# Kernel optimization log

Hardware: AMD Instinct MI355X
Metric: run time of the kernel (lower is better)

The kernel has to match this reference:

```python
import jax, jax.numpy as jnp
import numpy as np

N, K, A, P = 8192, 32, 5, 64
RBF_BINS = 16
D_MIN, D_MAX = 0.0, 22.0
REL_CLIP = 32


def _rbf(d, d_min=D_MIN, d_max=D_MAX, bins=RBF_BINS):
    centers = jnp.linspace(d_min, d_max, bins)
    sigma = (d_max - d_min) / bins
    return jnp.exp(-(((d[..., None] - centers) / sigma) ** 2))


def _frames(pos):
    # pos: [N, A, 3]; atoms 0=N, 1=CA, 2=C -> Gram-Schmidt backbone frame
    t = pos[:, 1]
    v1 = pos[:, 2] - t
    v2 = pos[:, 0] - t
    e1 = v1 / (jnp.linalg.norm(v1, axis=-1, keepdims=True) + 1e-6)
    u2 = v2 - (v2 * e1).sum(-1, keepdims=True) * e1
    e2 = u2 / (jnp.linalg.norm(u2, axis=-1, keepdims=True) + 1e-6)
    e3 = jnp.cross(e1, e2)
    R = jnp.stack([e1, e2, e3], axis=-1)  # [N,3,3], columns are basis vectors
    return R, t


def setup_inputs() -> dict:
    key = jax.random.key(0)
    ks = jax.random.split(key, 20)
    pos = jax.random.normal(ks[0], (N, A, 3), dtype=jnp.float32) * 3.0
    dmap = jax.random.uniform(ks[1], (N, N), dtype=jnp.float32) * 30.0
    neighbours = jax.random.randint(ks[2], (N, K), 0, N)
    resi = jax.random.randint(ks[3], (N,), 0, 512)
    chain = jnp.sort(jax.random.randint(ks[4], (N,), 0, 4))
    batch = jnp.sort(jax.random.randint(ks[5], (N,), 0, 8))
    mask = jnp.ones((N,), jnp.float32)

    def lin(k, fan_in, fan_out):
        return jax.random.normal(k, (fan_in, fan_out), dtype=jnp.float32) / np.sqrt(fan_in)

    REL = 2 * REL_CLIP + 1
    params = dict(
        W_rel=lin(ks[6], REL, P),
        W_dmap=lin(ks[7], RBF_BINS, P),
        W_dist=lin(ks[8], A * A * RBF_BINS, P),
        W_dir=lin(ks[9], A * 3, P),
        W_rot=lin(ks[10], 9, P),
        W_vec=lin(ks[11], A * 3, P),
        ln_g=jnp.ones((P,), jnp.float32),
        ln_b=jnp.zeros((P,), jnp.float32),
        W1=lin(ks[12], P, 2 * P),
        b1=jnp.zeros((2 * P,), jnp.float32),
        W2=lin(ks[13], 2 * P, P),
        b2=jnp.zeros((P,), jnp.float32),
    )
    return dict(pos=pos, dmap=dmap, neighbours=neighbours, resi=resi,
                chain=chain, batch=batch, mask=mask, **params)


def reference(pos, dmap, neighbours, resi, chain, batch, mask,
              W_rel, W_dmap, W_dist, W_dir, W_rot, W_vec,
              ln_g, ln_b, W1, b1, W2, b2):
    idx = jnp.clip(neighbours, 0, None)                     # safe gather for -1 padding
    nb_valid = (neighbours != -1).astype(mask.dtype)
    pair_mask = mask[:, None] * mask[idx] * nb_valid        # [N,K]

    # --- sequence relative position (one-hot, masked to same chain & batch) ---
    rel = jnp.clip(resi[idx] - resi[:, None], -REL_CLIP, REL_CLIP) + REL_CLIP
    same = ((chain[idx] == chain[:, None]) & (batch[idx] == batch[:, None]))
    rel_feat = jax.nn.one_hot(rel, 2 * REL_CLIP + 1, dtype=pos.dtype) * same[..., None].astype(pos.dtype)
    pair = jnp.einsum('nkf,fp->nkp', rel_feat, W_rel)

    # --- gathered distance-map branch ---
    dmap_nb = dmap[jnp.arange(N)[:, None], idx]             # [N,K]
    dmap_feat = jnp.where(pair_mask[..., None] > 0, _rbf(dmap_nb), 0.0)
    pair += jnp.einsum('nkf,fp->nkp', dmap_feat, W_dmap)

    # --- geometric features from frames ---
    R, t = _frames(pos)                                     # [N,3,3], [N,3]
    pos_j = pos[idx]                                        # [N,K,A,3]

    # all-atom pairwise distances residue i vs neighbour j: [N,K,A,A]
    d = jnp.linalg.norm(pos[:, None, :, None, :] - pos_j[:, :, None, :, :], axis=-1)
    dist_feat = _rbf(d).reshape(N, K, A * A * RBF_BINS)
    pair += jnp.einsum('nkf,fp->nkp', dist_feat, W_dist)

    # neighbour atoms in local frame of residue i: R_i^T (x - t_i)
    rel_vec = jnp.einsum('nji,nkaj->nkai', R, pos_j - t[:, None, None, :])  # [N,K,A,3]
    dirs = rel_vec / (jnp.linalg.norm(rel_vec, axis=-1, keepdims=True) + 1e-6)
    pair += jnp.einsum('nkf,fp->nkp', dirs.reshape(N, K, A * 3), W_dir)
    pair += jnp.einsum('nkf,fp->nkp', (rel_vec / 10.0).reshape(N, K, A * 3), W_vec)

    # relative rotation R_i^T R_j flattened: [N,K,9]
    rot = jnp.einsum('nji,nkjl->nkil', R, R[idx]).reshape(N, K, 9)
    pair += jnp.einsum('nkf,fp->nkp', rot, W_rot)

    # --- LayerNorm ---
    mu = pair.mean(-1, keepdims=True)
    var = ((pair - mu) ** 2).mean(-1, keepdims=True)
    pair = ln_g * (pair - mu) / jnp.sqrt(var + 1e-5) + ln_b

    # --- MLP (2P hidden, gelu) ---
    h = jax.nn.gelu(jnp.einsum('nkp,ph->nkh', pair, W1) + b1)
    pair = jnp.einsum('nkh,hp->nkp', h, W2) + b2
    return pair, pair_mask
```

## Files before the change

### kernel.cpp

```cpp
#include <hip/hip_runtime.h>
#include <cstdint>
#include <cstddef>

#define NN 8192
#define KK 32

typedef __bf16 bf16x8 __attribute__((ext_vector_type(8)));
typedef float  f32x4  __attribute__((ext_vector_type(4)));

union U4B { uint4 u; bf16x8 h; };
__device__ __forceinline__ bf16x8 asbf(uint4 u){ U4B v; v.u = u; return v.h; }

__device__ __forceinline__ unsigned short ftobf16(float f){
  union { float f; unsigned int i; } v; v.f = f;
  unsigned int x = v.i;
  x += 0x7fffu + ((x >> 16) & 1u);
  return (unsigned short)(x >> 16);
}
__device__ __forceinline__ float fast_gelu(float x){
  float y = 0.7978845608028654f * (x + 0.044715f * x * x * x);
  float e = __expf(2.0f * y);
  float t = 1.0f - 2.0f / (e + 1.0f);
  return 0.5f * x * (1.0f + t);
}

struct Frame { float e[9]; float t[3]; };
__device__ __forceinline__ Frame calc_frame(const float* p){
  Frame fr;
  float tx=p[3], ty=p[4], tz=p[5];
  float v1x=p[6]-tx, v1y=p[7]-ty, v1z=p[8]-tz;
  float v2x=p[0]-tx, v2y=p[1]-ty, v2z=p[2]-tz;
  float n1 = sqrtf(v1x*v1x+v1y*v1y+v1z*v1z) + 1e-6f;
  float e1x=v1x/n1, e1y=v1y/n1, e1z=v1z/n1;
  float dp = v2x*e1x+v2y*e1y+v2z*e1z;
  float ux=v2x-dp*e1x, uy=v2y-dp*e1y, uz=v2z-dp*e1z;
  float n2 = sqrtf(ux*ux+uy*uy+uz*uz) + 1e-6f;
  float e2x=ux/n2, e2y=uy/n2, e2z=uz/n2;
  fr.e[0]=e1x; fr.e[1]=e1y; fr.e[2]=e1z;
  fr.e[3]=e2x; fr.e[4]=e2y; fr.e[5]=e2z;
  fr.e[6]=e1y*e2z - e1z*e2y;
  fr.e[7]=e1z*e2x - e1x*e2z;
  fr.e[8]=e1x*e2y - e1y*e2x;
  fr.t[0]=tx; fr.t[1]=ty; fr.t[2]=tz;
  return fr;
}

__global__ void prep_w(const float* __restrict__ W_dmap, const float* __restrict__ W_dist,
    const float* __restrict__ W_dir, const float* __restrict__ W_rot,
    const float* __restrict__ W_vec, const float* __restrict__ W1,
    const float* __restrict__ W2, unsigned short* __restrict__ ws)
{
  int idx = blockIdx.x*256 + threadIdx.x;
  if (idx < 64*488){
    int p = idx / 488, k = idx - p*488;
    float v = 0.0f;
    if      (k < 400) v = W_dist[k*64+p];
    else if (k < 416) v = W_dmap[(k-400)*64+p];
    else if (k < 431) v = W_dir[(k-416)*64+p];
    else if (k < 446) v = W_vec[(k-431)*64+p];
    else if (k < 455) v = W_rot[(k-446)*64+p];
    ws[idx] = ftobf16(v);
  } else if (idx < 64*488 + 128*64){
    int i = idx - 64*488; int j = i>>6, p = i&63;
    ws[idx] = ftobf16(W1[p*128+j]);
  } else if (idx < 64*488 + 128*64 + 64*128){
    int i = idx - (64*488 + 128*64); int p = i>>7, j = i&127;
    ws[idx] = ftobf16(W2[j*64+p]);
  }
}

__global__ __launch_bounds__(256, 2)
void dsd_mfma(const float* __restrict__ pos, const float* __restrict__ dmap,
    const int* __restrict__ nbr, const int* __restrict__ resi,
    const int* __restrict__ chain, const int* __restrict__ batch,
    const float* __restrict__ mask,
    const float* __restrict__ W_rel,
    const float* __restrict__ ln_g, const float* __restrict__ ln_b,
    const float* __restrict__ b1, const float* __restrict__ b2,
    const unsigned short* __restrict__ wt,
    const unsigned short* __restrict__ w1t,
    const unsigned short* __restrict__ w2t,
    float* __restrict__ out)
{
  __shared__ __align__(16) unsigned short sFeat[32][488];
  __shared__ __align__(16) unsigned short sXA[32][72];
  __shared__ __align__(16) unsigned short sH[32][136];
  __shared__ __align__(16) float x32[32][68];
  __shared__ float sPosJ[32][16];
  __shared__ float sD[32][25];
  __shared__ float sPosI[15];
  __shared__ float sFrN[12];
  __shared__ float sLnG[64], sLnB[64], sB1[128], sB2[64];
  __shared__ int   sJ[32], sRel[32];
  __shared__ float sSame[32], sPm[32], sDv[32];

  const int tid  = threadIdx.x;
  const int w    = tid >> 6;
  const int lane = tid & 63;
  const int l15  = lane & 15;
  const int q    = lane >> 4;
  const int n    = blockIdx.x;
  const int mt   = w & 1;
  const int ng   = w >> 1;

  uint4 pB[15];
  {
    const unsigned short* rowp = wt + (size_t)(w*16 + l15)*488 + q*8;
    #pragma unroll
    for (int kk=0; kk<15; ++kk) pB[kk] = *(const uint4*)(rowp + kk*32);
  }
  uint4 b1B[4][2];
  #pragma unroll
  for (int t=0;t<4;++t){
    const unsigned short* rowp = w1t + (size_t)((ng*4+t)*16 + l15)*64 + q*8;
    #pragma unroll
    for (int kk=0;kk<2;++kk) b1B[t][kk] = *(const uint4*)(rowp + kk*32);
  }
  uint4 b2B[2][4];
  #pragma unroll
  for (int t=0;t<2;++t){
    const unsigned short* rowp = w2t + (size_t)((ng*2+t)*16 + l15)*128 + q*8;
    #pragma unroll
    for (int kk=0;kk<4;++kk) b2B[t][kk] = *(const uint4*)(rowp + kk*32);
  }

  if (tid < 32){
    int nb = nbr[n*KK + tid];
    int valid = (nb != -1) ? 1 : 0;
    int j = nb < 0 ? 0 : nb;
    sJ[tid] = j;
    int rl = resi[j] - resi[n];
    rl = rl < -32 ? -32 : (rl > 32 ? 32 : rl);
    sRel[tid] = rl + 32;
    sSame[tid] = (chain[j]==chain[n] && batch[j]==batch[n]) ? 1.0f : 0.0f;
    float pm = mask[n]*mask[j]*(float)valid;
    sPm[tid] = pm;
    sDv[tid] = dmap[(size_t)n*NN + j];
    out[(size_t)NN*KK*64 + (size_t)n*KK + tid] = pm;
  } else if (tid < 47){
    sPosI[tid-32] = pos[n*15 + (tid-32)];
  } else if (tid == 47){
    float pl[9];
    #pragma unroll
    for (int i=0;i<9;++i) pl[i] = pos[n*15+i];
    Frame fr = calc_frame(pl);
    #pragma unroll
    for (int i=0;i<9;++i) sFrN[i] = fr.e[i];
    #pragma unroll
    for (int i=0;i<3;++i) sFrN[9+i] = fr.t[i];
  } else if (tid >= 64 && tid < 192){
    sB1[tid-64] = b1[tid-64];
  } else if (tid >= 192){
    sB2[tid-192] = b2[tid-192];
  }
  if (tid < 64){ sLnG[tid] = ln_g[tid]; sLnB[tid] = ln_b[tid]; }
  __syncthreads();

  #pragma unroll
  for (int t=0;t<2;++t){
    int e = tid + t*256;
    int pair = e >> 4, qq = e & 15;
    if (qq < 15) sPosJ[pair][qq] = pos[sJ[pair]*15 + qq];
  }
  float wr0[4], wr1[4];
  #pragma unroll
  for (int r=0;r<4;++r){
    int p0 = q*4+r, p1 = 16+q*4+r;
    int pc = w*16 + l15;
    wr0[r] = (sSame[p0] != 0.0f) ? W_rel[sRel[p0]*64 + pc] : 0.0f;
    wr1[r] = (sSame[p1] != 0.0f) ? W_rel[sRel[p1]*64 + pc] : 0.0f;
  }
  __syncthreads();

  {
    int pair = tid >> 3, a = tid & 7;
    if (a < 5){
      float x0 = sPosJ[pair][a*3+0] - sFrN[9];
      float x1 = sPosJ[pair][a*3+1] - sFrN[10];
      float x2 = sPosJ[pair][a*3+2] - sFrN[11];
      float r0 = sFrN[0]*x0 + sFrN[1]*x1 + sFrN[2]*x2;
      float r1 = sFrN[3]*x0 + sFrN[4]*x1 + sFrN[5]*x2;
      float r2 = sFrN[6]*x0 + sFrN[7]*x1 + sFrN[8]*x2;
      float inv = 1.0f/(sqrtf(r0*r0+r1*r1+r2*r2)+1e-6f);
      sFeat[pair][416+a*3+0] = ftobf16(r0*inv);
      sFeat[pair][416+a*3+1] = ftobf16(r1*inv);
      sFeat[pair][416+a*3+2] = ftobf16(r2*inv);
      sFeat[pair][431+a*3+0] = ftobf16(r0*0.1f);
      sFeat[pair][431+a*3+1] = ftobf16(r1*0.1f);
      sFeat[pair][431+a*3+2] = ftobf16(r2*0.1f);
    }
  }
  if (tid < 32){
    Frame fj = calc_frame(sPosJ[tid]);
    #pragma unroll
    for (int i=0;i<3;++i)
      #pragma unroll
      for (int l=0;l<3;++l)
        sFeat[tid][446+i*3+l] = ftobf16(
          sFrN[i*3+0]*fj.e[l*3+0] + sFrN[i*3+1]*fj.e[l*3+1] + sFrN[i*3+2]*fj.e[l*3+2]);
  }
  #pragma unroll
  for (int t=0;t<4;++t){
    int e = tid + t*256;
    int pair = e >> 5, ab = e & 31;
    if (ab < 25){
      int a = ab/5, b = ab - (ab/5)*5;
      float dx = sPosI[a*3+0] - sPosJ[pair][b*3+0];
      float dy = sPosI[a*3+1] - sPosJ[pair][b*3+1];
      float dz = sPosI[a*3+2] - sPosJ[pair][b*3+2];
      sD[pair][ab] = sqrtf(dx*dx+dy*dy+dz*dz);
      sFeat[pair][455+ab] = 0;
    }
  }
  __syncthreads();

  for (int t=0;t<25;++t){
    int e = tid + t*256;
    int pair = e / 200;
    int rem  = e - pair*200;
    int ab = rem >> 3, cp = rem & 7;
    float d = sD[pair][ab];
    float z0 = (d - (float)(2*cp  )*(22.0f/15.0f)) * (1.0f/1.375f);
    float z1 = (d - (float)(2*cp+1)*(22.0f/15.0f)) * (1.0f/1.375f);
    unsigned int u0 = ftobf16(__expf(-z0*z0));
    unsigned int u1 = ftobf16(__expf(-z1*z1));
    *(unsigned int*)&sFeat[pair][ab*16 + cp*2] = u0 | (u1<<16);
  }
  #pragma unroll
  for (int t=0;t<2;++t){
    int e = tid + t*256;
    int pair = e >> 4, c = e & 15;
    float z = (sDv[pair] - (float)c*(22.0f/15.0f)) * (1.0f/1.375f);
    float v = (sPm[pair] > 0.0f) ? __expf(-z*z) : 0.0f;
    sFeat[pair][400+c] = ftobf16(v);
  }
  __syncthreads();

  f32x4 acc0 = {0.f,0.f,0.f,0.f}, acc1 = {0.f,0.f,0.f,0.f};
  {
    const unsigned short* a0p = &sFeat[l15][q*8];
    const unsigned short* a1p = &sFeat[16+l15][q*8];
    #pragma unroll
    for (int kk=0; kk<15; ++kk){
      bf16x8 A0 = asbf(*(const uint4*)(a0p + kk*32));
      bf16x8 A1 = asbf(*(const uint4*)(a1p + kk*32));
      bf16x8 B  = asbf(pB[kk]);
      acc0 = __builtin_amdgcn_mfma_f32_16x16x32_bf16(A0, B, acc0, 0,0,0);
      acc1 = __builtin_amdgcn_mfma_f32_16x16x32_bf16(A1, B, acc1, 0,0,0);
    }
  }
  {
    int pc = w*16 + l15;
    #pragma unroll
    for (int r=0;r<4;++r){
      x32[q*4+r][pc]    = acc0[r] + wr0[r];
      x32[16+q*4+r][pc] = acc1[r] + wr1[r];
    }
  }
  __syncthreads();

  {
    int pair = tid >> 3, g = tid & 7;
    float4 xa = *(const float4*)&x32[pair][g*8];
    float4 xb = *(const float4*)&x32[pair][g*8+4];
    float vals[8] = {xa.x,xa.y,xa.z,xa.w, xb.x,xb.y,xb.z,xb.w};
    float s = 0.f, s2 = 0.f;
    #pragma unroll
    for (int i=0;i<8;++i){ s += vals[i]; s2 += vals[i]*vals[i]; }
    #pragma unroll
    for (int o=1;o<8;o<<=1){ s += __shfl_xor(s,o,64); s2 += __shfl_xor(s2,o,64); }
    float mu  = s  * (1.0f/64.0f);
    float var = s2 * (1.0f/64.0f) - mu*mu;
    float inv = rsqrtf(var + 1e-5f);
    unsigned int pk[4];
    #pragma unroll
    for (int i=0;i<4;++i){
      int p0 = g*8 + 2*i;
      float v0 = sLnG[p0  ]*(vals[2*i  ]-mu)*inv + sLnB[p0  ];
      float v1 = sLnG[p0+1]*(vals[2*i+1]-mu)*inv + sLnB[p0+1];
      pk[i] = (unsigned int)ftobf16(v0) | ((unsigned int)ftobf16(v1)<<16);
    }
    uint4 pkv; pkv.x=pk[0]; pkv.y=pk[1]; pkv.z=pk[2]; pkv.w=pk[3];
    *(uint4*)&sXA[pair][g*8] = pkv;
  }
  __syncthreads();

  f32x4 hacc[4];
  #pragma unroll
  for (int t=0;t<4;++t){ hacc[t][0]=0.f; hacc[t][1]=0.f; hacc[t][2]=0.f; hacc[t][3]=0.f; }
  {
    const unsigned short* ap = &sXA[mt*16 + l15][q*8];
    #pragma unroll
    for (int kk=0;kk<2;++kk){
      bf16x8 A = asbf(*(const uint4*)(ap + kk*32));
      #pragma unroll
      for (int t=0;t<4;++t)
        hacc[t] = __builtin_amdgcn_mfma_f32_16x16x32_bf16(A, asbf(b1B[t][kk]), hacc[t], 0,0,0);
    }
  }
  #pragma unroll
  for (int t=0;t<4;++t){
    int j = (ng*4+t)*16 + l15;
    float bb = sB1[j];
    #pragma unroll
    for (int r=0;r<4;++r){
      int m = mt*16 + q*4 + r;
      sH[m][j] = ftobf16(fast_gelu(hacc[t][r] + bb));
    }
  }
  __syncthreads();

  f32x4 oacc[2];
  #pragma unroll
  for (int t=0;t<2;++t){ oacc[t][0]=0.f; oacc[t][1]=0.f; oacc[t][2]=0.f; oacc[t][3]=0.f; }
  {
    const unsigned short* ap = &sH[mt*16 + l15][q*8];
    #pragma unroll
    for (int kk=0;kk<4;++kk){
      bf16x8 A = asbf(*(const uint4*)(ap + kk*32));
      #pragma unroll
      for (int t=0;t<2;++t)
        oacc[t] = __builtin_amdgcn_mfma_f32_16x16x32_bf16(A, asbf(b2B[t][kk]), oacc[t], 0,0,0);
    }
  }
  #pragma unroll
  for (int t=0;t<2;++t){
    int p = (ng*2+t)*16 + l15;
    float bb = sB2[p];
    #pragma unroll
    for (int r=0;r<4;++r){
      int m = mt*16 + q*4 + r;
      out[((size_t)n*KK + m)*64 + p] = oacc[t][r] + bb;
    }
  }
}

extern "C" void kernel_launch(void* const* d_in, const int* in_sizes, int n_in,
                              void* d_out, int out_size, void* d_ws, size_t ws_size,
                              hipStream_t stream) {
  (void)in_sizes; (void)n_in; (void)out_size; (void)ws_size;
  const float* pos    = (const float*)d_in[0];
  const float* dmap   = (const float*)d_in[1];
  const int*   nbr    = (const int*)  d_in[2];
  const int*   resi   = (const int*)  d_in[3];
  const int*   chain  = (const int*)  d_in[4];
  const int*   batch  = (const int*)  d_in[5];
  const float* mask   = (const float*)d_in[6];
  const float* W_rel  = (const float*)d_in[7];
  const float* W_dmap = (const float*)d_in[8];
  const float* W_dist = (const float*)d_in[9];
  const float* W_dir  = (const float*)d_in[10];
  const float* W_rot  = (const float*)d_in[11];
  const float* W_vec  = (const float*)d_in[12];
  const float* ln_g   = (const float*)d_in[13];
  const float* ln_b   = (const float*)d_in[14];
  const float* W1     = (const float*)d_in[15];
  const float* b1     = (const float*)d_in[16];
  const float* W2     = (const float*)d_in[17];
  const float* b2     = (const float*)d_in[18];
  float* out = (float*)d_out;

  unsigned short* wt  = (unsigned short*)d_ws;
  unsigned short* w1t = wt + 64*488;
  unsigned short* w2t = w1t + 128*64;

  prep_w<<<dim3(186), dim3(256), 0, stream>>>(W_dmap, W_dist, W_dir, W_rot, W_vec, W1, W2, wt);
  dsd_mfma<<<dim3(NN), dim3(256), 0, stream>>>(
      pos, dmap, nbr, resi, chain, batch, mask, W_rel,
      ln_g, ln_b, b1, b2, wt, w1t, w2t, out);
}
```

Measured before the change: 551.4 us.

## Alias LDS buffers, defer MLP weight loads, fuse LayerNorm into MFMA registers

Reduces LDS footprint by aliasing sXA/sH onto sFeat and removing x32 and the LN gamma/beta arrays, and raises launch bounds from 2 to 4 blocks per CU. W1/W2 fragments are now loaded after the first GEMM, which shortens their register live range. LayerNorm statistics are reduced by cross-lane shuffles directly on the MFMA accumulators, with one small partial-sum exchange through shared memory, instead of a round trip through a float staging buffer. The RBF expansion is restructured to use exp2 with prefolded constants and packed bf16 conversion, and the neighbour position gather is folded into the first phase, removing one barrier. Risks are register spills under the tighter launch bound and aliasing hazards when sFeat is reused.

```diff
diff --git a/kernel.cpp b/kernel.cpp
--- a/kernel.cpp
+++ b/kernel.cpp
@@ -1,4 +1,5 @@
 #include <hip/hip_runtime.h>
+#include <hip/hip_bf16.h>
 #include <cstdint>
 #include <cstddef>
 
@@ -16,6 +17,18 @@
   unsigned int x = v.i;
   x += 0x7fffu + ((x >> 16) & 1u);
   return (unsigned short)(x >> 16);
+}
+__device__ __forceinline__ unsigned int pk_bf16(float a, float b){
+  union { __hip_bfloat162 h; unsigned int u; } v;
+  v.h = __float22bfloat162_rn(float2{a, b});
+  return v.u;
+}
+__device__ __forceinline__ float exp2n(float u){
+#if __has_builtin(__builtin_amdgcn_exp2f)
+  return __builtin_amdgcn_exp2f(-u);
+#else
+  return exp2f(-u);
+#endif
 }
 __device__ __forceinline__ float fast_gelu(float x){
   float y = 0.7978845608028654f * (x + 0.044715f * x * x * x);
@@ -69,7 +82,10 @@
   }
 }
 
-__global__ __launch_bounds__(256, 2)
+#define RBF_K1 0.8735435700f
+#define RBF_K2 1.2811972361f
+
+__global__ __launch_bounds__(256, 4)
 void dsd_mfma(const float* __restrict__ pos, const float* __restrict__ dmap,
     const int* __restrict__ nbr, const int* __restrict__ resi,
     const int* __restrict__ chain, const int* __restrict__ batch,
@@ -83,16 +99,18 @@
     float* __restrict__ out)
 {
   __shared__ __align__(16) unsigned short sFeat[32][488];
-  __shared__ __align__(16) unsigned short sXA[32][72];
-  __shared__ __align__(16) unsigned short sH[32][136];
-  __shared__ __align__(16) float x32[32][68];
-  __shared__ float sPosJ[32][16];
+  __shared__ __align__(16) float2 sLNp[32][4];
+  __shared__ __align__(16) float sPosJ[32][16];
   __shared__ float sD[32][25];
   __shared__ float sPosI[15];
   __shared__ float sFrN[12];
-  __shared__ float sLnG[64], sLnB[64], sB1[128], sB2[64];
-  __shared__ int   sJ[32], sRel[32];
+  __shared__ float sB1[128];
+  __shared__ float sB2[64];
+  __shared__ int   sRel[32];
   __shared__ float sSame[32], sPm[32], sDv[32];
+
+  unsigned short (*sXA)[72]  = (unsigned short(*)[72])(&sFeat[0][0]);
+  unsigned short (*sH)[136]  = (unsigned short(*)[136])(&sFeat[0][0] + 2304);
 
   const int tid  = threadIdx.x;
   const int w    = tid >> 6;
@@ -102,33 +120,23 @@
   const int n    = blockIdx.x;
   const int mt   = w & 1;
   const int ng   = w >> 1;
+  const int g    = tid & 7;
+  const int pairD= tid >> 3;
+
+  const float lng = ln_g[w*16 + l15];
+  const float lnb = ln_b[w*16 + l15];
 
   uint4 pB[15];
   {
     const unsigned short* rowp = wt + (size_t)(w*16 + l15)*488 + q*8;
     #pragma unroll
     for (int kk=0; kk<15; ++kk) pB[kk] = *(const uint4*)(rowp + kk*32);
-  }
-  uint4 b1B[4][2];
-  #pragma unroll
-  for (int t=0;t<4;++t){
-    const unsigned short* rowp = w1t + (size_t)((ng*4+t)*16 + l15)*64 + q*8;
-    #pragma unroll
-    for (int kk=0;kk<2;++kk) b1B[t][kk] = *(const uint4*)(rowp + kk*32);
-  }
-  uint4 b2B[2][4];
-  #pragma unroll
-  for (int t=0;t<2;++t){
-    const unsigned short* rowp = w2t + (size_t)((ng*2+t)*16 + l15)*128 + q*8;
-    #pragma unroll
-    for (int kk=0;kk<4;++kk) b2B[t][kk] = *(const uint4*)(rowp + kk*32);
   }
 
   if (tid < 32){
     int nb = nbr[n*KK + tid];
     int valid = (nb != -1) ? 1 : 0;
     int j = nb < 0 ? 0 : nb;
-    sJ[tid] = j;
     int rl = resi[j] - resi[n];
     rl = rl < -32 ? -32 : (rl > 32 ? 32 : rl);
     sRel[tid] = rl + 32;
@@ -137,6 +145,9 @@
     sPm[tid] = pm;
     sDv[tid] = dmap[(size_t)n*NN + j];
     out[(size_t)NN*KK*64 + (size_t)n*KK + tid] = pm;
+    const float* pj = pos + (size_t)j*15;
+    #pragma unroll
+    for (int qq=0; qq<15; ++qq) sPosJ[tid][qq] = pj[qq];
   } else if (tid < 47){
     sPosI[tid-32] = pos[n*15 + (tid-32)];
   } else if (tid == 47){
@@ -153,42 +164,34 @@
   } else if (tid >= 192){
     sB2[tid-192] = b2[tid-192];
   }
-  if (tid < 64){ sLnG[tid] = ln_g[tid]; sLnB[tid] = ln_b[tid]; }
-  __syncthreads();
-
-  #pragma unroll
-  for (int t=0;t<2;++t){
-    int e = tid + t*256;
-    int pair = e >> 4, qq = e & 15;
-    if (qq < 15) sPosJ[pair][qq] = pos[sJ[pair]*15 + qq];
-  }
+  __syncthreads();
+
   float wr0[4], wr1[4];
-  #pragma unroll
-  for (int r=0;r<4;++r){
-    int p0 = q*4+r, p1 = 16+q*4+r;
+  {
     int pc = w*16 + l15;
-    wr0[r] = (sSame[p0] != 0.0f) ? W_rel[sRel[p0]*64 + pc] : 0.0f;
-    wr1[r] = (sSame[p1] != 0.0f) ? W_rel[sRel[p1]*64 + pc] : 0.0f;
-  }
-  __syncthreads();
-
-  {
-    int pair = tid >> 3, a = tid & 7;
-    if (a < 5){
-      float x0 = sPosJ[pair][a*3+0] - sFrN[9];
-      float x1 = sPosJ[pair][a*3+1] - sFrN[10];
-      float x2 = sPosJ[pair][a*3+2] - sFrN[11];
-      float r0 = sFrN[0]*x0 + sFrN[1]*x1 + sFrN[2]*x2;
-      float r1 = sFrN[3]*x0 + sFrN[4]*x1 + sFrN[5]*x2;
-      float r2 = sFrN[6]*x0 + sFrN[7]*x1 + sFrN[8]*x2;
-      float inv = 1.0f/(sqrtf(r0*r0+r1*r1+r2*r2)+1e-6f);
-      sFeat[pair][416+a*3+0] = ftobf16(r0*inv);
-      sFeat[pair][416+a*3+1] = ftobf16(r1*inv);
-      sFeat[pair][416+a*3+2] = ftobf16(r2*inv);
-      sFeat[pair][431+a*3+0] = ftobf16(r0*0.1f);
-      sFeat[pair][431+a*3+1] = ftobf16(r1*0.1f);
-      sFeat[pair][431+a*3+2] = ftobf16(r2*0.1f);
-    }
+    #pragma unroll
+    for (int r=0;r<4;++r){
+      int p0 = q*4+r, p1 = 16+q*4+r;
+      wr0[r] = sSame[p0] * W_rel[sRel[p0]*64 + pc];
+      wr1[r] = sSame[p1] * W_rel[sRel[p1]*64 + pc];
+    }
+  }
+
+  if (g < 5){
+    int a = g;
+    float x0 = sPosJ[pairD][a*3+0] - sFrN[9];
+    float x1 = sPosJ[pairD][a*3+1] - sFrN[10];
+    float x2 = sPosJ[pairD][a*3+2] - sFrN[11];
+    float r0 = sFrN[0]*x0 + sFrN[1]*x1 + sFrN[2]*x2;
+    float r1 = sFrN[3]*x0 + sFrN[4]*x1 + sFrN[5]*x2;
+    float r2 = sFrN[6]*x0 + sFrN[7]*x1 + sFrN[8]*x2;
+    float inv = 1.0f/(sqrtf(r0*r0+r1*r1+r2*r2)+1e-6f);
+    sFeat[pairD][416+a*3+0] = ftobf16(r0*inv);
+    sFeat[pairD][416+a*3+1] = ftobf16(r1*inv);
+    sFeat[pairD][416+a*3+2] = ftobf16(r2*inv);
+    sFeat[pairD][431+a*3+0] = ftobf16(r0*0.1f);
+    sFeat[pairD][431+a*3+1] = ftobf16(r1*0.1f);
+    sFeat[pairD][431+a*3+2] = ftobf16(r2*0.1f);
   }
   if (tid < 32){
     Frame fj = calc_frame(sPosJ[tid]);
@@ -214,25 +217,21 @@
   }
   __syncthreads();
 
-  for (int t=0;t<25;++t){
-    int e = tid + t*256;
-    int pair = e / 200;
-    int rem  = e - pair*200;
-    int ab = rem >> 3, cp = rem & 7;
-    float d = sD[pair][ab];
-    float z0 = (d - (float)(2*cp  )*(22.0f/15.0f)) * (1.0f/1.375f);
-    float z1 = (d - (float)(2*cp+1)*(22.0f/15.0f)) * (1.0f/1.375f);
-    unsigned int u0 = ftobf16(__expf(-z0*z0));
-    unsigned int u1 = ftobf16(__expf(-z1*z1));
-    *(unsigned int*)&sFeat[pair][ab*16 + cp*2] = u0 | (u1<<16);
-  }
-  #pragma unroll
-  for (int t=0;t<2;++t){
-    int e = tid + t*256;
-    int pair = e >> 4, c = e & 15;
-    float z = (sDv[pair] - (float)c*(22.0f/15.0f)) * (1.0f/1.375f);
-    float v = (sPm[pair] > 0.0f) ? __expf(-z*z) : 0.0f;
-    sFeat[pair][400+c] = ftobf16(v);
+  {
+    const float c0k = (float)(2*g  ) * RBF_K2;
+    const float c1k = (float)(2*g+1) * RBF_K2;
+    unsigned short* frow = &sFeat[pairD][2*g];
+    #pragma unroll
+    for (int t=0;t<25;++t){
+      float dp = sD[pairD][t] * RBF_K1;
+      float w0 = dp - c0k, w1 = dp - c1k;
+      *(unsigned int*)(frow + t*16) = pk_bf16(exp2n(w0*w0), exp2n(w1*w1));
+    }
+    float dp = sDv[pairD] * RBF_K1;
+    float w0 = dp - c0k, w1 = dp - c1k;
+    float e0 = exp2n(w0*w0), e1 = exp2n(w1*w1);
+    if (!(sPm[pairD] > 0.0f)){ e0 = 0.0f; e1 = 0.0f; }
+    *(unsigned int*)(frow + 400) = pk_bf16(e0, e1);
   }
   __syncthreads();
 
@@ -249,39 +248,73 @@
       acc1 = __builtin_amdgcn_mfma_f32_16x16x32_bf16(A1, B, acc1, 0,0,0);
     }
   }
-  {
-    int pc = w*16 + l15;
+  #pragma unroll
+  for (int r=0;r<4;++r){ acc0[r] += wr0[r]; acc1[r] += wr1[r]; }
+
+  uint4 b1B[4][2];
+  #pragma unroll
+  for (int t=0;t<4;++t){
+    const unsigned short* rowp = w1t + (size_t)((ng*4+t)*16 + l15)*64 + q*8;
+    #pragma unroll
+    for (int kk=0;kk<2;++kk) b1B[t][kk] = *(const uint4*)(rowp + kk*32);
+  }
+  uint4 b2B[2][4];
+  #pragma unroll
+  for (int t=0;t<2;++t){
+    const unsigned short* rowp = w2t + (size_t)((ng*2+t)*16 + l15)*128 + q*8;
+    #pragma unroll
+    for (int kk=0;kk<4;++kk) b2B[t][kk] = *(const uint4*)(rowp + kk*32);
+  }
+
+  {
+    float s0[4], v0[4], s1[4], v1[4];
     #pragma unroll
     for (int r=0;r<4;++r){
-      x32[q*4+r][pc]    = acc0[r] + wr0[r];
-      x32[16+q*4+r][pc] = acc1[r] + wr1[r];
-    }
-  }
-  __syncthreads();
-
-  {
-    int pair = tid >> 3, g = tid & 7;
-    float4 xa = *(const float4*)&x32[pair][g*8];
-    float4 xb = *(const float4*)&x32[pair][g*8+4];
-    float vals[8] = {xa.x,xa.y,xa.z,xa.w, xb.x,xb.y,xb.z,xb.w};
-    float s = 0.f, s2 = 0.f;
-    #pragma unroll
-    for (int i=0;i<8;++i){ s += vals[i]; s2 += vals[i]*vals[i]; }
-    #pragma unroll
-    for (int o=1;o<8;o<<=1){ s += __shfl_xor(s,o,64); s2 += __shfl_xor(s2,o,64); }
-    float mu  = s  * (1.0f/64.0f);
-    float var = s2 * (1.0f/64.0f) - mu*mu;
-    float inv = rsqrtf(var + 1e-5f);
-    unsigned int pk[4];
-    #pragma unroll
-    for (int i=0;i<4;++i){
-      int p0 = g*8 + 2*i;
-      float v0 = sLnG[p0  ]*(vals[2*i  ]-mu)*inv + sLnB[p0  ];
-      float v1 = sLnG[p0+1]*(vals[2*i+1]-mu)*inv + sLnB[p0+1];
-      pk[i] = (unsigned int)ftobf16(v0) | ((unsigned int)ftobf16(v1)<<16);
-    }
-    uint4 pkv; pkv.x=pk[0]; pkv.y=pk[1]; pkv.z=pk[2]; pkv.w=pk[3];
-    *(uint4*)&sXA[pair][g*8] = pkv;
+      s0[r]=acc0[r]; v0[r]=acc0[r]*acc0[r];
+      s1[r]=acc1[r]; v1[r]=acc1[r]*acc1[r];
+    }
+    #pragma unroll
+    for (int off=1; off<16; off<<=1){
+      #pragma unroll
+      for (int r=0;r<4;++r){
+        s0[r] += __shfl_xor(s0[r], off, 64);
+        v0[r] += __shfl_xor(v0[r], off, 64);
+        s1[r] += __shfl_xor(s1[r], off, 64);
+        v1[r] += __shfl_xor(v1[r], off, 64);
+      }
+    }
+    if (l15 == 0){
+      #pragma unroll
+      for (int r=0;r<4;++r){
+        sLNp[q*4+r][w]    = float2{s0[r], v0[r]};
+        sLNp[16+q*4+r][w] = float2{s1[r], v1[r]};
+      }
+    }
+  }
+  __syncthreads();
+
+  #pragma unroll
+  for (int r=0;r<4;++r){
+    {
+      int m = q*4+r;
+      float4 pa = *(const float4*)&sLNp[m][0];
+      float4 pb = *(const float4*)&sLNp[m][2];
+      float s  = pa.x + pa.z + pb.x + pb.z;
+      float s2 = pa.y + pa.w + pb.y + pb.w;
+      float mu = s * (1.0f/64.0f);
+      float inv = rsqrtf(s2*(1.0f/64.0f) - mu*mu + 1e-5f);
+      sXA[m][w*16 + l15] = ftobf16(lng*(acc0[r]-mu)*inv + lnb);
+    }
+    {
+      int m = 16+q*4+r;
+      float4 pa = *(const float4*)&sLNp[m][0];
+      float4 pb = *(const float4*)&sLNp[m][2];
+      float s  = pa.x + pa.z + pb.x + pb.z;
+      float s2 = pa.y + pa.w + pb.y + pb.w;
+      float mu = s * (1.0f/64.0f);
+      float inv = rsqrtf(s2*(1.0f/64.0f) - mu*mu + 1e-5f);
+      sXA[m][w*16 + l15] = ftobf16(lng*(acc1[r]-mu)*inv + lnb);
+    }
   }
   __syncthreads();
 
```

New measurement: 466.8 us. -15.3%, faster.
